# Optimization experiments

Measured on AMD Instinct MI355X. Metric: run time of the kernel, lower is better.

## Reference

```python
import jax, jax.numpy as jnp
import numpy as np

B, L, D = 2, 2048, 2048
H, Hd = 16, 128


def _rotary_cos_sin(max_len, dim, base=10000.0):
    inv_freq = 1.0 / (base ** (np.arange(0, dim, 2, dtype=np.float32) / dim))
    t = np.arange(max_len, dtype=np.float32)
    freqs = np.outer(t, inv_freq)                      # [L, dim/2]
    emb = np.concatenate([freqs, freqs], axis=-1)      # [L, dim]
    cos = np.cos(emb)[None, None]                      # [1,1,L,dim]
    sin = np.sin(emb)[None, None]
    return jnp.asarray(cos), jnp.asarray(sin)


def setup_inputs() -> dict:
    key = jax.random.key(0)
    ks = jax.random.split(key, 5)
    hidden_states = jax.random.normal(ks[0], (B, L, D), dtype=jnp.float32)
    cos, sin = _rotary_cos_sin(L, Hd)
    s = 1.0 / np.sqrt(D)
    wq = jax.random.normal(ks[1], (H * Hd, D), dtype=jnp.float32) * s
    wk = jax.random.normal(ks[2], (H * Hd, D), dtype=jnp.float32) * s
    wv = jax.random.normal(ks[3], (H * Hd, D), dtype=jnp.float32) * s
    wo = jax.random.normal(ks[4], (D, H * Hd), dtype=jnp.float32) * s
    return {"hidden_states": hidden_states, "cos": cos, "sin": sin,
            "wq": wq, "wk": wk, "wv": wv, "wo": wo}


def _rotate_half(x):
    x1, x2 = jnp.split(x, 2, axis=-1)
    return jnp.concatenate([-x2, x1], axis=-1)


def reference(hidden_states, cos, sin, wq, wk, wv, wo):
    b, l, d = hidden_states.shape
    # QKV projections -> [B, H, L, Hd]
    q = (hidden_states @ wq.T).reshape(b, l, H, Hd).transpose(0, 2, 1, 3)
    k = (hidden_states @ wk.T).reshape(b, l, H, Hd).transpose(0, 2, 1, 3)
    v = (hidden_states @ wv.T).reshape(b, l, H, Hd).transpose(0, 2, 1, 3)
    c = cos[:, :, :l, :]
    s = sin[:, :, :l, :]
    q = q * c + _rotate_half(q) * s
    k = k * c + _rotate_half(k) * s
    # SDPA (non-causal, default scale = 1/sqrt(head_dim))
    scale = 1.0 / jnp.sqrt(jnp.asarray(Hd, dtype=q.dtype))
    scores = jnp.einsum('bhqd,bhkd->bhqk', q, k) * scale
    attn = jax.nn.softmax(scores, axis=-1)
    out = jnp.einsum('bhqk,bhkd->bhqd', attn, v)       # [B,H,L,Hd]
    out = out.transpose(0, 2, 1, 3).reshape(b, l, H * Hd)
    return out @ wo.T
```

## Files before the change

kernel.cpp:

```cpp
#include <hip/hip_runtime.h>

constexpr int Bb = 2;
constexpr int Ll = 2048;
constexpr int Dd = 2048;
constexpr int Hh = 16;
constexpr int Hd = 128;
constexpr int M  = Bb * Ll;

typedef __attribute__((ext_vector_type(8)))  short s16x8;
typedef __attribute__((ext_vector_type(4)))  float f32x4;
typedef __attribute__((ext_vector_type(16))) float f32x16;

__device__ __forceinline__ unsigned short f2bf(float f) {
    union { float f; unsigned u; } v; v.f = f;
    unsigned r = v.u + 0x7fffu + ((v.u >> 16) & 1u);
    return (unsigned short)(r >> 16);
}
__device__ __forceinline__ float bf2f(unsigned short b) {
    union { unsigned u; float f; } v; v.u = ((unsigned)b) << 16;
    return v.f;
}
__device__ __forceinline__ float fast_exp2(float x) {
#if __has_builtin(__builtin_amdgcn_exp2f)
    return __builtin_amdgcn_exp2f(x);
#else
    return exp2f(x);
#endif
}

__device__ __forceinline__ void gld16(const void* g, void* l) {
#if __has_builtin(__builtin_amdgcn_global_load_lds)
    __builtin_amdgcn_global_load_lds(
        (const __attribute__((address_space(1))) unsigned int*)g,
        (__attribute__((address_space(3))) unsigned int*)l, 16, 0, 0);
#else
    int lane = threadIdx.x & 63;
    ((int4*)l)[lane] = ((const int4*)g)[0];
#endif
}

__global__ __launch_bounds__(256)
void f2bf_all(const float* __restrict__ x,  const float* __restrict__ wq,
              const float* __restrict__ wk, const float* __restrict__ wv,
              const float* __restrict__ wo,
              unsigned short* __restrict__ Xb,  unsigned short* __restrict__ Wqb,
              unsigned short* __restrict__ Wkb, unsigned short* __restrict__ Wvb,
              unsigned short* __restrict__ Wob)
{
    int bid = blockIdx.x;
    const float* in; unsigned short* out; int off;
    if      (bid <  8192) { in = x;  out = Xb;  off = bid; }
    else if (bid < 12288) { in = wq; out = Wqb; off = bid - 8192; }
    else if (bid < 16384) { in = wk; out = Wkb; off = bid - 12288; }
    else if (bid < 20480) { in = wv; out = Wvb; off = bid - 16384; }
    else                  { in = wo; out = Wob; off = bid - 20480; }
    int i = (off * 256 + threadIdx.x) * 4;
    float4 v = *(const float4*)(in + i);
    ushort4 o;
    o.x = f2bf(v.x); o.y = f2bf(v.y); o.z = f2bf(v.z); o.w = f2bf(v.w);
    *(ushort4*)(out + i) = o;
}

__global__ __launch_bounds__(256, 2)
void mfma_gemm_qkv(const unsigned short* __restrict__ A,
                   const unsigned short* __restrict__ Wall,
                   unsigned short* __restrict__ Oq,
                   unsigned short* __restrict__ Ok,
                   unsigned short* __restrict__ Ov)
{
    constexpr int K  = 2048;
    constexpr int NT = K / 64;
    constexpr int BM = 128, BN = 192;
    constexpr int SLOT_US = (BM + BN) * 64;

    __shared__ unsigned short lds[2 * SLOT_US];

    const int t    = threadIdx.x;
    const int w    = t >> 6, lane = t & 63;
    const int wm   = w >> 1, wn = w & 1;
    const int m0   = blockIdx.y * BM, n0 = blockIdx.x * BN;
    const int r16  = lane & 15, q4 = lane >> 4;
    const int lxor = (r16 & 7) << 4;

    const int srow8 = lane >> 3;
    const int sgcol = (((lane & 7) ^ srow8) << 4);
    const char* Agb = (const char*)A;
    const char* Wgb = (const char*)Wall;

    f32x4 acc[4][6];
#pragma unroll
    for (int i = 0; i < 4; ++i)
#pragma unroll
        for (int j = 0; j < 6; ++j)
            acc[i][j] = (f32x4){0.f, 0.f, 0.f, 0.f};

#define STAGE_ALL(tt, sl) do {                                               \
    _Pragma("unroll") for (int p = 0; p < 4; ++p) {                          \
        int ia_ = w * 4 + p;                                                 \
        gld16(Agb + (size_t)(m0 + ia_ * 8 + srow8) * (K * 2) + (tt) * 128 + sgcol, \
              &lds[(sl) * SLOT_US + ia_ * 512]);                             \
    }                                                                        \
    _Pragma("unroll") for (int p = 0; p < 6; ++p) {                          \
        int ib_ = w * 6 + p;                                                 \
        gld16(Wgb + (size_t)(n0 + ib_ * 8 + srow8) * (K * 2) + (tt) * 128 + sgcol, \
              &lds[(sl) * SLOT_US + BM * 64 + ib_ * 512]);                   \
    }                                                                        \
} while (0)

#define MFMA24() do {                                                        \
    __builtin_amdgcn_s_setprio(1);                                           \
    _Pragma("unroll") for (int mi = 0; mi < 4; ++mi)                         \
    _Pragma("unroll") for (int ni = 0; ni < 6; ++ni)                         \
        acc[mi][ni] = __builtin_amdgcn_mfma_f32_16x16x32_bf16(                \
            a[mi], b[ni], acc[mi][ni], 0, 0, 0);                             \
    __builtin_amdgcn_s_setprio(0);                                           \
} while (0)

    STAGE_ALL(0, 0);
    asm volatile("s_waitcnt vmcnt(0)" ::: "memory");
    __builtin_amdgcn_s_barrier();
    asm volatile("" ::: "memory");

    for (int tt = 0; tt < NT; ++tt) {
        const int slot = tt & 1;
        const char* Ab = (const char*)&lds[slot * SLOT_US];
        const char* Bp = (const char*)&lds[slot * SLOT_US + BM * 64];
        const int c0 = (q4 * 16) ^ lxor;
        const int c1 = (64 + q4 * 16) ^ lxor;

        s16x8 a[4], b[6];

#pragma unroll
        for (int mi = 0; mi < 4; ++mi)
            a[mi] = *(const s16x8*)(Ab + (wm * 64 + mi * 16 + r16) * 128 + c0);
#pragma unroll
        for (int ni = 0; ni < 6; ++ni)
            b[ni] = *(const s16x8*)(Bp + (wn * 96 + ni * 16 + r16) * 128 + c0);
        if (tt + 1 < NT) STAGE_ALL(tt + 1, slot ^ 1);
        MFMA24();

#pragma unroll
        for (int mi = 0; mi < 4; ++mi)
            a[mi] = *(const s16x8*)(Ab + (wm * 64 + mi * 16 + r16) * 128 + c1);
#pragma unroll
        for (int ni = 0; ni < 6; ++ni)
            b[ni] = *(const s16x8*)(Bp + (wn * 96 + ni * 16 + r16) * 128 + c1);
        MFMA24();

        asm volatile("s_waitcnt vmcnt(0)" ::: "memory");
        __builtin_amdgcn_s_barrier();
        asm volatile("" ::: "memory");
    }
#undef STAGE_ALL
#undef MFMA24

#pragma unroll
    for (int ni = 0; ni < 6; ++ni) {
        int nb   = n0 + wn * 96 + ni * 16;
        int nsel = nb >> 11;
        int nr   = nb & 2047;
        int h    = nr >> 7;
        int d    = (nr & 127) + r16;
        if (nsel < 2) {
            unsigned short* O = nsel ? Ok : Oq;
#pragma unroll
            for (int mi = 0; mi < 4; ++mi)
#pragma unroll
                for (int r = 0; r < 4; ++r) {
                    int m = m0 + wm * 64 + mi * 16 + q4 * 4 + r;
                    int b = m >> 11, l = m & 2047;
                    O[(((size_t)b * Hh + h) * Ll + l) * Hd + d] =
                        f2bf(acc[mi][ni][r]);
                }
        } else {
#pragma unroll
            for (int mi = 0; mi < 4; ++mi) {
                int mb = m0 + wm * 64 + mi * 16 + q4 * 4;
                int b = mb >> 11, l = mb & 2047;
                ushort4 pk;
                pk.x = f2bf(acc[mi][ni][0]);
                pk.y = f2bf(acc[mi][ni][1]);
                pk.z = f2bf(acc[mi][ni][2]);
                pk.w = f2bf(acc[mi][ni][3]);
                *(ushort4*)&Ov[(((size_t)b * Hh + h) * Hd + d) * Ll + l] = pk;
            }
        }
    }
}

__global__ __launch_bounds__(512, 2)
void mfma_gemm_out(const unsigned short* __restrict__ A,
                   const unsigned short* __restrict__ W,
                   float* __restrict__ FO)
{
    constexpr int K  = 2048;
    constexpr int NT = K / 64;
    constexpr int SLOT_US = 24576;

    __shared__ unsigned short lds[3 * SLOT_US];

    const int t    = threadIdx.x;
    const int w    = t >> 6, lane = t & 63;
    const int wm   = w >> 1, wn = w & 1;
    const int m0   = blockIdx.y * 256, n0 = blockIdx.x * 128;
    const int r16  = lane & 15, q4 = lane >> 4;
    const int lxor = (r16 & 7) << 4;

    const int srow8 = lane >> 3;
    const int sgcol = (((lane & 7) ^ srow8) << 4);
    const char* Agb = (const char*)A;
    const char* Wgb = (const char*)W;

    f32x4 acc[4][4];
#pragma unroll
    for (int i = 0; i < 4; ++i)
#pragma unroll
        for (int j = 0; j < 4; ++j)
            acc[i][j] = (f32x4){0.f, 0.f, 0.f, 0.f};

    s16x8 af[4], bf[4];

#define STAGE_A(tt, sl, p) do {                                              \
    int ia_ = w * 4 + (p);                                                   \
    gld16(Agb + (size_t)(m0 + ia_ * 8 + srow8) * (K * 2) + (tt) * 128 + sgcol, \
          &lds[(sl) * SLOT_US + ia_ * 512]); } while (0)
#define STAGE_B(tt, sl, p) do {                                              \
    int ib_ = w * 2 + (p);                                                   \
    gld16(Wgb + (size_t)(n0 + ib_ * 8 + srow8) * (K * 2) + (tt) * 128 + sgcol, \
          &lds[(sl) * SLOT_US + 16384 + ib_ * 512]); } while (0)

#define LOAD_FRAGS(sl, ksub) do {                                            \
    const char* Ab_ = (const char*)&lds[(sl) * SLOT_US];                     \
    const char* Bb_ = (const char*)&lds[(sl) * SLOT_US + 16384];             \
    int cc_ = ((ksub) * 64 + q4 * 16) ^ lxor;                                \
    _Pragma("unroll") for (int mi = 0; mi < 4; ++mi)                         \
        af[mi] = *(const s16x8*)(Ab_ + (wm * 64 + mi * 16 + r16) * 128 + cc_); \
    _Pragma("unroll") for (int ni = 0; ni < 4; ++ni)                         \
        bf[ni] = *(const s16x8*)(Bb_ + (wn * 64 + ni * 16 + r16) * 128 + cc_); \
} while (0)

#define DO_MFMA() do {                                                       \
    __builtin_amdgcn_s_setprio(1);                                           \
    _Pragma("unroll") for (int mi = 0; mi < 4; ++mi)                         \
    _Pragma("unroll") for (int ni = 0; ni < 4; ++ni)                         \
        acc[mi][ni] = __builtin_amdgcn_mfma_f32_16x16x32_bf16(                \
            af[mi], bf[ni], acc[mi][ni], 0, 0, 0);                           \
    __builtin_amdgcn_s_setprio(0);                                           \
} while (0)

    STAGE_A(0, 0, 0); STAGE_A(0, 0, 1); STAGE_B(0, 0, 0);
    STAGE_A(0, 0, 2); STAGE_A(0, 0, 3); STAGE_B(0, 0, 1);
    STAGE_A(1, 1, 0); STAGE_A(1, 1, 1); STAGE_B(1, 1, 0);
    STAGE_A(1, 1, 2); STAGE_A(1, 1, 3); STAGE_B(1, 1, 1);
    asm volatile("s_waitcnt vmcnt(6)" ::: "memory");
    __builtin_amdgcn_s_barrier();
    asm volatile("" ::: "memory");

    int slot = 0;
    for (int tt = 0; tt < NT; ++tt) {
        int snx = slot + 2; if (snx >= 3) snx -= 3;
        const bool pf = (tt + 2 < NT);

        LOAD_FRAGS(slot, 0);
        if (pf) { STAGE_A(tt + 2, snx, 0); STAGE_A(tt + 2, snx, 1); STAGE_B(tt + 2, snx, 0); }
        asm volatile("" ::: "memory");
        __builtin_amdgcn_s_barrier();
        asm volatile("s_waitcnt lgkmcnt(0)" ::: "memory");
        DO_MFMA();
        asm volatile("" ::: "memory");
        __builtin_amdgcn_s_barrier();
        asm volatile("" ::: "memory");

        LOAD_FRAGS(slot, 1);
        if (pf) { STAGE_A(tt + 2, snx, 2); STAGE_A(tt + 2, snx, 3); STAGE_B(tt + 2, snx, 1); }
        asm volatile("" ::: "memory");
        __builtin_amdgcn_s_barrier();
        asm volatile("s_waitcnt lgkmcnt(0)" ::: "memory");
        DO_MFMA();
        if (pf)               asm volatile("s_waitcnt vmcnt(6)" ::: "memory");
        else if (tt + 1 < NT) asm volatile("s_waitcnt vmcnt(0)" ::: "memory");
        asm volatile("" ::: "memory");
        __builtin_amdgcn_s_barrier();
        asm volatile("" ::: "memory");

        slot = (slot == 2) ? 0 : slot + 1;
    }
#undef STAGE_A
#undef STAGE_B
#undef LOAD_FRAGS
#undef DO_MFMA

#pragma unroll
    for (int mi = 0; mi < 4; ++mi)
#pragma unroll
        for (int ni = 0; ni < 4; ++ni) {
            int n = n0 + wn * 64 + ni * 16 + r16;
#pragma unroll
            for (int r = 0; r < 4; ++r) {
                int m = m0 + wm * 64 + mi * 16 + q4 * 4 + r;
                FO[(size_t)m * Dd + n] = acc[mi][ni][r];
            }
        }
}

__global__ __launch_bounds__(256)
void rope_bf16(unsigned short* __restrict__ q, unsigned short* __restrict__ k,
               const float* __restrict__ cosb, const float* __restrict__ sinb)
{
    const float QS = 0.1275175f;
    const int t = threadIdx.x;
    int rblk = blockIdx.x;
    unsigned short* base;
    float sc;
    if (rblk < 4096) { base = q; sc = QS; }
    else             { base = k; sc = 1.0f; rblk -= 4096; }

    const int row = rblk * 16 + (t >> 4);
    const int l   = row & (Ll - 1);
    const int d0  = (t & 15) * 8;
    unsigned short* xr = base + (size_t)row * Hd;

    s16x8 v0 = *(const s16x8*)(xr + d0);
    s16x8 vp = *(const s16x8*)(xr + (d0 ^ 64));
    const float* cp = cosb + (size_t)l * Hd + d0;
    const float* sp = sinb + (size_t)l * Hd + d0;
    float4 c0 = *(const float4*)cp,       c1 = *(const float4*)(cp + 4);
    float4 sa = *(const float4*)sp,       sb = *(const float4*)(sp + 4);
    const float cc[8] = {c0.x, c0.y, c0.z, c0.w, c1.x, c1.y, c1.z, c1.w};
    const float ss[8] = {sa.x, sa.y, sa.z, sa.w, sb.x, sb.y, sb.z, sb.w};
    const float sgn = (d0 < 64) ? -1.f : 1.f;

    s16x8 o;
#pragma unroll
    for (int j = 0; j < 8; ++j) {
        float a = bf2f((unsigned short)v0[j]);
        float p = bf2f((unsigned short)vp[j]);
        float res = fmaf(a, cc[j], sgn * p * ss[j]) * sc;
        o[j] = (short)f2bf(res);
    }
    asm volatile("" ::: "memory");
    *(s16x8*)(xr + d0) = o;
}

__global__ __launch_bounds__(256)
void flash_attn(const unsigned short* __restrict__ q,
                const unsigned short* __restrict__ k,
                const unsigned short* __restrict__ vT,
                unsigned short* __restrict__ ctx)
{
    __shared__ unsigned short Ks[2][64 * 128];
    __shared__ unsigned short Vs[2][128 * 64];
    __shared__ unsigned short Ps[4][32 * 64];

    const int t = threadIdx.x;
    const int w = t >> 6, lane = t & 63;
    const int n32 = lane & 31, half = lane >> 5;
    const int bh = blockIdx.x >> 4;
    const int l0 = (blockIdx.x & 15) * 128;

    const unsigned short* qb = q  + ((size_t)bh * Ll + l0 + w * 32) * Hd;
    const unsigned short* kb = k  + (size_t)bh * Ll * Hd;
    const unsigned short* vb = vT + (size_t)bh * Hd * Ll;

    const int k_r = lane >> 4, k_u = lane & 15;
    const int v_r = lane >> 3, v_u = lane & 7;

#define STAGE(J0, bsel) do {                                                  \
    _Pragma("unroll") for (int p = 0; p < 4; ++p) {                           \
        int j_ = w * 4 + p;                                                   \
        int row_ = j_ * 4 + k_r;                                              \
        gld16(kb + (size_t)((J0) + row_) * Hd + ((k_u ^ (row_ & 7)) * 8),     \
              &Ks[bsel][j_ * 512]);                                           \
    }                                                                         \
    _Pragma("unroll") for (int p = 0; p < 4; ++p) {                           \
        int j_ = w * 4 + p;                                                   \
        int row_ = j_ * 8 + v_r;                                              \
        gld16(vb + (size_t)row_ * Ll + (J0) + ((v_u ^ (row_ & 7)) * 8),       \
              &Vs[bsel][j_ * 512]);                                           \
    }                                                                         \
} while (0)

    s16x8 qf[8];
#pragma unroll
    for (int ks = 0; ks < 8; ++ks)
        qf[ks] = *(const s16x8*)(qb + (size_t)n32 * Hd + ks * 16 + half * 8);

    f32x16 o[4];
    float lacc[16];
#pragma unroll
    for (int nt = 0; nt < 4; ++nt)
#pragma unroll
        for (int r = 0; r < 16; ++r) o[nt][r] = 0.f;
#pragma unroll
    for (int r = 0; r < 16; ++r) lacc[r] = 0.f;

    unsigned short* Pw = Ps[w];
    const int psw = (n32 & 7) << 3;

    STAGE(0, 0);
    __syncthreads();

    int buf = 0;
    for (int j0 = 0; j0 < Ll; j0 += 64) {
        if (j0 + 64 < Ll) STAGE(j0 + 64, buf ^ 1);

        f32x16 s0, s1;
#pragma unroll
        for (int r = 0; r < 16; ++r) { s0[r] = 0.f; s1[r] = 0.f; }
        __builtin_amdgcn_s_setprio(1);
#pragma unroll
        for (int ks = 0; ks < 8; ++ks) {
            int kc = (ks * 16 + half * 8) ^ psw;
            s16x8 b0 = *(const s16x8*)&Ks[buf][n32 * 128 + kc];
            s16x8 b1 = *(const s16x8*)&Ks[buf][(32 + n32) * 128 + kc];
            s0 = __builtin_amdgcn_mfma_f32_32x32x16_bf16(qf[ks], b0, s0, 0, 0, 0);
            s1 = __builtin_amdgcn_mfma_f32_32x32x16_bf16(qf[ks], b1, s1, 0, 0, 0);
        }
        __builtin_amdgcn_s_setprio(0);

#pragma unroll
        for (int r = 0; r < 16; ++r) {
            int mrow = (r & 3) + 8 * (r >> 2) + 4 * half;
            int sw = (mrow & 7) << 3;
            float p0 = fast_exp2(s0[r]);
            float p1 = fast_exp2(s1[r]);
            lacc[r] += p0 + p1;
            union { float f; unsigned u; } u0, u1;
            u0.f = p0; u1.f = p1;
            Pw[mrow * 64 + (n32 ^ sw)]        = (unsigned short)((u0.u + 0x8000u) >> 16);
            Pw[mrow * 64 + ((32 + n32) ^ sw)] = (unsigned short)((u1.u + 0x8000u) >> 16);
        }

        __builtin_amdgcn_s_setprio(1);
#pragma unroll
        for (int kst = 0; kst < 4; ++kst) {
            int cc = (kst * 16 + half * 8) ^ psw;
            s16x8 pf2 = *(const s16x8*)&Pw[n32 * 64 + cc];
#pragma unroll
            for (int nt = 0; nt < 4; ++nt) {
                s16x8 vf = *(const s16x8*)&Vs[buf][(nt * 32 + n32) * 64 + cc];
                o[nt] = __builtin_amdgcn_mfma_f32_32x32x16_bf16(pf2, vf, o[nt], 0, 0, 0);
            }
        }
        __builtin_amdgcn_s_setprio(0);

        __syncthreads();
        buf ^= 1;
    }
#undef STAGE

    float linv[16];
#pragma unroll
    for (int r = 0; r < 16; ++r) {
        float s = lacc[r];
        s += __shfl_xor(s, 1, 64);
        s += __shfl_xor(s, 2, 64);
        s += __shfl_xor(s, 4, 64);
        s += __shfl_xor(s, 8, 64);
        s += __shfl_xor(s, 16, 64);
        linv[r] = 1.0f / s;
    }

    const int b = bh >> 4, h = bh & 15;
#pragma unroll
    for (int nt = 0; nt < 4; ++nt)
#pragma unroll
        for (int r = 0; r < 16; ++r) {
            int mrow = (r & 3) + 8 * (r >> 2) + 4 * half;
            int lq = l0 + w * 32 + mrow;
            ctx[((size_t)(b * Ll + lq)) * Dd + h * Hd + nt * 32 + n32] =
                f2bf(o[nt][r] * linv[r]);
        }
}

extern "C" void kernel_launch(void* const* d_in, const int* in_sizes, int n_in,
                              void* d_out, int out_size, void* d_ws, size_t ws_size,
                              hipStream_t stream)
{
    const float* hs   = (const float*)d_in[0];
    const float* cosb = (const float*)d_in[1];
    const float* sinb = (const float*)d_in[2];
    const float* wq   = (const float*)d_in[3];
    const float* wk   = (const float*)d_in[4];
    const float* wv   = (const float*)d_in[5];
    const float* wo   = (const float*)d_in[6];
    float* out = (float*)d_out;

    char* ws = (char*)d_ws;
    unsigned short* Xb  = (unsigned short*)(ws);
    unsigned short* Wqb = (unsigned short*)(ws + (16ull << 20));
    unsigned short* Wkb = (unsigned short*)(ws + (24ull << 20));
    unsigned short* Wvb = (unsigned short*)(ws + (32ull << 20));
    unsigned short* Wob = (unsigned short*)(ws + (40ull << 20));
    unsigned short* qb  = (unsigned short*)(ws + (48ull << 20));
    unsigned short* kb  = (unsigned short*)(ws + (64ull << 20));
    unsigned short* vTb = (unsigned short*)(ws + (80ull << 20));
    unsigned short* ctx = Xb;

    f2bf_all<<<dim3(24576), dim3(256), 0, stream>>>(
        hs, wq, wk, wv, wo, Xb, Wqb, Wkb, Wvb, Wob);

    mfma_gemm_qkv<<<dim3(6144 / 192, M / 128), dim3(256), 0, stream>>>(
        Xb, Wqb, qb, kb, vTb);

    rope_bf16<<<dim3(2 * (Bb * Hh * Ll) / 16), dim3(256), 0, stream>>>(
        qb, kb, cosb, sinb);

    flash_attn<<<dim3(Bb * Hh * (Ll / 128)), dim3(256), 0, stream>>>(qb, kb, vTb, ctx);

    mfma_gemm_out<<<dim3(Dd / 128, M / 256), dim3(512), 0, stream>>>(
        ctx, Wob, out);
}
```

Measured before the change: 386.2 us.

## Load QKV GEMM A fragments directly from global into registers, drop A LDS staging

The QKV projection GEMM no longer stages the activation tile through LDS. Each wave now loads its A fragments straight from global memory into double-buffered registers one tile ahead, and only the weight tile goes through LDS. This shrinks LDS per block and raises the launch-bounds occupancy hint from 2 to 3 blocks, and the barrier wait now only covers the B-tile loads (vmcnt(8)). The trade-off is higher register pressure from the two sets of 8 A fragments, and global loads that are less coalesced, with each lane reading 16-byte pieces spread across rows.

```diff
diff --git a/kernel.cpp b/kernel.cpp
--- a/kernel.cpp
+++ b/kernel.cpp
@@ -61,7 +61,7 @@
     *(ushort4*)(out + i) = o;
 }
 
-__global__ __launch_bounds__(256, 2)
+__global__ __launch_bounds__(256, 3)
 void mfma_gemm_qkv(const unsigned short* __restrict__ A,
                    const unsigned short* __restrict__ Wall,
                    unsigned short* __restrict__ Oq,
@@ -71,7 +71,7 @@
     constexpr int K  = 2048;
     constexpr int NT = K / 64;
     constexpr int BM = 128, BN = 192;
-    constexpr int SLOT_US = (BM + BN) * 64;
+    constexpr int SLOT_US = BN * 64;
 
     __shared__ unsigned short lds[2 * SLOT_US];
 
@@ -87,6 +87,9 @@
     const char* Agb = (const char*)A;
     const char* Wgb = (const char*)Wall;
 
+    const int c0 = (q4 * 16) ^ lxor;
+    const int c1 = (64 + q4 * 16) ^ lxor;
+
     f32x4 acc[4][6];
 #pragma unroll
     for (int i = 0; i < 4; ++i)
@@ -94,65 +97,70 @@
         for (int j = 0; j < 6; ++j)
             acc[i][j] = (f32x4){0.f, 0.f, 0.f, 0.f};
 
-#define STAGE_ALL(tt, sl) do {                                               \
-    _Pragma("unroll") for (int p = 0; p < 4; ++p) {                          \
-        int ia_ = w * 4 + p;                                                 \
-        gld16(Agb + (size_t)(m0 + ia_ * 8 + srow8) * (K * 2) + (tt) * 128 + sgcol, \
-              &lds[(sl) * SLOT_US + ia_ * 512]);                             \
-    }                                                                        \
+#define STAGE_B(tt, sl) do {                                                 \
     _Pragma("unroll") for (int p = 0; p < 6; ++p) {                          \
         int ib_ = w * 6 + p;                                                 \
         gld16(Wgb + (size_t)(n0 + ib_ * 8 + srow8) * (K * 2) + (tt) * 128 + sgcol, \
-              &lds[(sl) * SLOT_US + BM * 64 + ib_ * 512]);                   \
+              &lds[(sl) * SLOT_US + ib_ * 512]);                             \
+    } } while (0)
+
+#define AFRAG_LOAD(dst, tt) do {                                             \
+    _Pragma("unroll") for (int mi = 0; mi < 4; ++mi) {                       \
+        const char* ap_ = Agb + (size_t)(m0 + wm * 64 + mi * 16 + r16) * (K * 2) \
+                          + (tt) * 128 + q4 * 16;                            \
+        dst[mi]     = *(const s16x8*)(ap_);                                  \
+        dst[4 + mi] = *(const s16x8*)(ap_ + 64);                             \
+    } } while (0)
+
+#define TILE(tt, aC, aN) do {                                                \
+    const int sl_ = (tt) & 1;                                                \
+    if ((tt) + 1 < NT) {                                                     \
+        STAGE_B((tt) + 1, sl_ ^ 1);                                          \
+        asm volatile("" ::: "memory");       \
+        AFRAG_LOAD(aN, (tt) + 1);                                            \
+        asm volatile("" ::: "memory");                                       \
     }                                                                        \
-} while (0)
-
-#define MFMA24() do {                                                        \
+    const char* Bp_ = (const char*)&lds[sl_ * SLOT_US];                      \
+    s16x8 bf_[6];                                                            \
+    _Pragma("unroll") for (int ni = 0; ni < 6; ++ni)                         \
+        bf_[ni] = *(const s16x8*)(Bp_ + (wn * 96 + ni * 16 + r16) * 128 + c0); \
     __builtin_amdgcn_s_setprio(1);                                           \
     _Pragma("unroll") for (int mi = 0; mi < 4; ++mi)                         \
     _Pragma("unroll") for (int ni = 0; ni < 6; ++ni)                         \
         acc[mi][ni] = __builtin_amdgcn_mfma_f32_16x16x32_bf16(                \
-            a[mi], b[ni], acc[mi][ni], 0, 0, 0);                             \
+            aC[mi], bf_[ni], acc[mi][ni], 0, 0, 0);                          \
     __builtin_amdgcn_s_setprio(0);                                           \
+    _Pragma("unroll") for (int ni = 0; ni < 6; ++ni)                         \
+        bf_[ni] = *(const s16x8*)(Bp_ + (wn * 96 + ni * 16 + r16) * 128 + c1); \
+    __builtin_amdgcn_s_setprio(1);                                           \
+    _Pragma("unroll") for (int mi = 0; mi < 4; ++mi)                         \
+    _Pragma("unroll") for (int ni = 0; ni < 6; ++ni)                         \
+        acc[mi][ni] = __builtin_amdgcn_mfma_f32_16x16x32_bf16(                \
+            aC[4 + mi], bf_[ni], acc[mi][ni], 0, 0, 0);                      \
+    __builtin_amdgcn_s_setprio(0);                                           \
+    if ((tt) + 1 < NT) {                                                     \
+        asm volatile("s_waitcnt vmcnt(8)" ::: "memory");   \
+        __builtin_amdgcn_s_barrier();                                        \
+        asm volatile("" ::: "memory");                                       \
+    }                                                                        \
 } while (0)
 
-    STAGE_ALL(0, 0);
+    s16x8 aA[8], aB[8];
+
+    STAGE_B(0, 0);
+    AFRAG_LOAD(aA, 0);
     asm volatile("s_waitcnt vmcnt(0)" ::: "memory");
     __builtin_amdgcn_s_barrier();
     asm volatile("" ::: "memory");
 
-    for (int tt = 0; tt < NT; ++tt) {
-        const int slot = tt & 1;
-        const char* Ab = (const char*)&lds[slot * SLOT_US];
-        const char* Bp = (const char*)&lds[slot * SLOT_US + BM * 64];
-        const int c0 = (q4 * 16) ^ lxor;
-        const int c1 = (64 + q4 * 16) ^ lxor;
-
-        s16x8 a[4], b[6];
-
-#pragma unroll
-        for (int mi = 0; mi < 4; ++mi)
-            a[mi] = *(const s16x8*)(Ab + (wm * 64 + mi * 16 + r16) * 128 + c0);
-#pragma unroll
-        for (int ni = 0; ni < 6; ++ni)
-            b[ni] = *(const s16x8*)(Bp + (wn * 96 + ni * 16 + r16) * 128 + c0);
-        if (tt + 1 < NT) STAGE_ALL(tt + 1, slot ^ 1);
-        MFMA24();
-
-#pragma unroll
-        for (int mi = 0; mi < 4; ++mi)
-            a[mi] = *(const s16x8*)(Ab + (wm * 64 + mi * 16 + r16) * 128 + c1);
-#pragma unroll
-        for (int ni = 0; ni < 6; ++ni)
-            b[ni] = *(const s16x8*)(Bp + (wn * 96 + ni * 16 + r16) * 128 + c1);
-        MFMA24();
-
-        asm volatile("s_waitcnt vmcnt(0)" ::: "memory");
-        __builtin_amdgcn_s_barrier();
-        asm volatile("" ::: "memory");
+#pragma unroll 1
+    for (int it = 0; it < NT; it += 2) {
+        TILE(it,     aA, aB);
+        TILE(it + 1, aB, aA);
     }
-#undef STAGE_ALL
-#undef MFMA24
+#undef STAGE_B
+#undef AFRAG_LOAD
+#undef TILE
 
 #pragma unroll
     for (int ni = 0; ni < 6; ++ni) {
```

Measured after the change: 959.6 us. 148% more time.

## Process two query tiles per wave in flash attention to reuse K/V

Applied to the files above, without the earlier changes.

Each wave now handles 64 query rows (two 32-row tiles) instead of 32, so every block covers 256 queries and the grid halves. Each K and V fragment read from LDS feeds twice as many MFMAs, and K/V global traffic per query is halved. In exchange register pressure roughly doubles (launch bounds set to 1 block per SM), the P scratch buffer grows, and only 256 blocks are launched, which may underfill the GPU's compute units.

```diff
diff --git a/kernel.cpp b/kernel.cpp
--- a/kernel.cpp
+++ b/kernel.cpp
@@ -342,7 +342,7 @@
     *(s16x8*)(xr + d0) = o;
 }
 
-__global__ __launch_bounds__(256)
+__global__ __launch_bounds__(256, 1)
 void flash_attn(const unsigned short* __restrict__ q,
                 const unsigned short* __restrict__ k,
                 const unsigned short* __restrict__ vT,
@@ -350,15 +350,15 @@
 {
     __shared__ unsigned short Ks[2][64 * 128];
     __shared__ unsigned short Vs[2][128 * 64];
-    __shared__ unsigned short Ps[4][32 * 64];
+    __shared__ unsigned short Ps[8][32 * 64];
 
     const int t = threadIdx.x;
     const int w = t >> 6, lane = t & 63;
     const int n32 = lane & 31, half = lane >> 5;
-    const int bh = blockIdx.x >> 4;
-    const int l0 = (blockIdx.x & 15) * 128;
-
-    const unsigned short* qb = q  + ((size_t)bh * Ll + l0 + w * 32) * Hd;
+    const int bh = blockIdx.x >> 3;
+    const int l0 = (blockIdx.x & 7) * 256;
+
+    const unsigned short* qb = q  + ((size_t)bh * Ll + l0) * Hd;
     const unsigned short* kb = k  + (size_t)bh * Ll * Hd;
     const unsigned short* vb = vT + (size_t)bh * Hd * Ll;
 
@@ -380,21 +380,24 @@
     }                                                                         \
 } while (0)
 
-    s16x8 qf[8];
-#pragma unroll
-    for (int ks = 0; ks < 8; ++ks)
-        qf[ks] = *(const s16x8*)(qb + (size_t)n32 * Hd + ks * 16 + half * 8);
-
-    f32x16 o[4];
-    float lacc[16];
+    s16x8 qf0[8], qf1[8];
+#pragma unroll
+    for (int ks = 0; ks < 8; ++ks) {
+        qf0[ks] = *(const s16x8*)(qb + (size_t)((w * 2 + 0) * 32 + n32) * Hd + ks * 16 + half * 8);
+        qf1[ks] = *(const s16x8*)(qb + (size_t)((w * 2 + 1) * 32 + n32) * Hd + ks * 16 + half * 8);
+    }
+
+    f32x16 o0[4], o1[4];
+    float la0[16], la1[16];
 #pragma unroll
     for (int nt = 0; nt < 4; ++nt)
 #pragma unroll
-        for (int r = 0; r < 16; ++r) o[nt][r] = 0.f;
-#pragma unroll
-    for (int r = 0; r < 16; ++r) lacc[r] = 0.f;
-
-    unsigned short* Pw = Ps[w];
+        for (int r = 0; r < 16; ++r) { o0[nt][r] = 0.f; o1[nt][r] = 0.f; }
+#pragma unroll
+    for (int r = 0; r < 16; ++r) { la0[r] = 0.f; la1[r] = 0.f; }
+
+    unsigned short* Pw0 = Ps[w * 2 + 0];
+    unsigned short* Pw1 = Ps[w * 2 + 1];
     const int psw = (n32 & 7) << 3;
 
     STAGE(0, 0);
@@ -404,17 +407,19 @@
     for (int j0 = 0; j0 < Ll; j0 += 64) {
         if (j0 + 64 < Ll) STAGE(j0 + 64, buf ^ 1);
 
-        f32x16 s0, s1;
-#pragma unroll
-        for (int r = 0; r < 16; ++r) { s0[r] = 0.f; s1[r] = 0.f; }
+        f32x16 s00, s01, s10, s11;
+#pragma unroll
+        for (int r = 0; r < 16; ++r) { s00[r] = 0.f; s01[r] = 0.f; s10[r] = 0.f; s11[r] = 0.f; }
         __builtin_amdgcn_s_setprio(1);
 #pragma unroll
         for (int ks = 0; ks < 8; ++ks) {
             int kc = (ks * 16 + half * 8) ^ psw;
             s16x8 b0 = *(const s16x8*)&Ks[buf][n32 * 128 + kc];
             s16x8 b1 = *(const s16x8*)&Ks[buf][(32 + n32) * 128 + kc];
-            s0 = __builtin_amdgcn_mfma_f32_32x32x16_bf16(qf[ks], b0, s0, 0, 0, 0);
-            s1 = __builtin_amdgcn_mfma_f32_32x32x16_bf16(qf[ks], b1, s1, 0, 0, 0);
+            s00 = __builtin_amdgcn_mfma_f32_32x32x16_bf16(qf0[ks], b0, s00, 0, 0, 0);
+            s01 = __builtin_amdgcn_mfma_f32_32x32x16_bf16(qf0[ks], b1, s01, 0, 0, 0);
+            s10 = __builtin_amdgcn_mfma_f32_32x32x16_bf16(qf1[ks], b0, s10, 0, 0, 0);
+            s11 = __builtin_amdgcn_mfma_f32_32x32x16_bf16(qf1[ks], b1, s11, 0, 0, 0);
         }
         __builtin_amdgcn_s_setprio(0);
 
@@ -422,24 +427,31 @@
         for (int r = 0; r < 16; ++r) {
             int mrow = (r & 3) + 8 * (r >> 2) + 4 * half;
             int sw = (mrow & 7) << 3;
-            float p0 = fast_exp2(s0[r]);
-            float p1 = fast_exp2(s1[r]);
-            lacc[r] += p0 + p1;
-            union { float f; unsigned u; } u0, u1;
-            u0.f = p0; u1.f = p1;
-            Pw[mrow * 64 + (n32 ^ sw)]        = (unsigned short)((u0.u + 0x8000u) >> 16);
-            Pw[mrow * 64 + ((32 + n32) ^ sw)] = (unsigned short)((u1.u + 0x8000u) >> 16);
+            float p00 = fast_exp2(s00[r]);
+            float p01 = fast_exp2(s01[r]);
+            float p10 = fast_exp2(s10[r]);
+            float p11 = fast_exp2(s11[r]);
+            la0[r] += p00 + p01;
+            la1[r] += p10 + p11;
+            union { float f; unsigned u; } u0, u1, u2, u3;
+            u0.f = p00; u1.f = p01; u2.f = p10; u3.f = p11;
+            Pw0[mrow * 64 + (n32 ^ sw)]        = (unsigned short)((u0.u + 0x8000u) >> 16);
+            Pw0[mrow * 64 + ((32 + n32) ^ sw)] = (unsigned short)((u1.u + 0x8000u) >> 16);
+            Pw1[mrow * 64 + (n32 ^ sw)]        = (unsigned short)((u2.u + 0x8000u) >> 16);
+            Pw1[mrow * 64 + ((32 + n32) ^ sw)] = (unsigned short)((u3.u + 0x8000u) >> 16);
         }
 
         __builtin_amdgcn_s_setprio(1);
 #pragma unroll
         for (int kst = 0; kst < 4; ++kst) {
             int cc = (kst * 16 + half * 8) ^ psw;
-            s16x8 pf2 = *(const s16x8*)&Pw[n32 * 64 + cc];
+            s16x8 pa = *(const s16x8*)&Pw0[n32 * 64 + cc];
+            s16x8 pb = *(const s16x8*)&Pw1[n32 * 64 + cc];
 #pragma unroll
             for (int nt = 0; nt < 4; ++nt) {
                 s16x8 vf = *(const s16x8*)&Vs[buf][(nt * 32 + n32) * 64 + cc];
-                o[nt] = __builtin_amdgcn_mfma_f32_32x32x16_bf16(pf2, vf, o[nt], 0, 0, 0);
+                o0[nt] = __builtin_amdgcn_mfma_f32_32x32x16_bf16(pa, vf, o0[nt], 0, 0, 0);
+                o1[nt] = __builtin_amdgcn_mfma_f32_32x32x16_bf16(pb, vf, o1[nt], 0, 0, 0);
             }
         }
         __builtin_amdgcn_s_setprio(0);
@@ -449,16 +461,23 @@
     }
 #undef STAGE
 
-    float linv[16];
+    float li0[16], li1[16];
 #pragma unroll
     for (int r = 0; r < 16; ++r) {
-        float s = lacc[r];
+        float s = la0[r];
         s += __shfl_xor(s, 1, 64);
         s += __shfl_xor(s, 2, 64);
         s += __shfl_xor(s, 4, 64);
         s += __shfl_xor(s, 8, 64);
         s += __shfl_xor(s, 16, 64);
-        linv[r] = 1.0f / s;
+        li0[r] = 1.0f / s;
+        float z = la1[r];
+        z += __shfl_xor(z, 1, 64);
+        z += __shfl_xor(z, 2, 64);
+        z += __shfl_xor(z, 4, 64);
+        z += __shfl_xor(z, 8, 64);
+        z += __shfl_xor(z, 16, 64);
+        li1[r] = 1.0f / z;
     }
 
     const int b = bh >> 4, h = bh & 15;
@@ -467,9 +486,12 @@
 #pragma unroll
         for (int r = 0; r < 16; ++r) {
             int mrow = (r & 3) + 8 * (r >> 2) + 4 * half;
-            int lq = l0 + w * 32 + mrow;
-            ctx[((size_t)(b * Ll + lq)) * Dd + h * Hd + nt * 32 + n32] =
-                f2bf(o[nt][r] * linv[r]);
+            int lq0 = l0 + (w * 2 + 0) * 32 + mrow;
+            int lq1 = l0 + (w * 2 + 1) * 32 + mrow;
+            ctx[((size_t)(b * Ll + lq0)) * Dd + h * Hd + nt * 32 + n32] =
+                f2bf(o0[nt][r] * li0[r]);
+            ctx[((size_t)(b * Ll + lq1)) * Dd + h * Hd + nt * 32 + n32] =
+                f2bf(o1[nt][r] * li1[r]);
         }
 }
 
@@ -506,7 +528,7 @@
     rope_bf16<<<dim3(2 * (Bb * Hh * Ll) / 16), dim3(256), 0, stream>>>(
         qb, kb, cosb, sinb);
 
-    flash_attn<<<dim3(Bb * Hh * (Ll / 128)), dim3(256), 0, stream>>>(qb, kb, vTb, ctx);
+    flash_attn<<<dim3(Bb * Hh * (Ll / 256)), dim3(256), 0, stream>>>(qb, kb, vTb, ctx);
 
     mfma_gemm_out<<<dim3(Dd / 128, M / 256), dim3(512), 0, stream>>>(
         ctx, Wob, out);
```

Result: slower. 408.7 us (+5.8%).

## Shrink output GEMM tile to 128x128 with double-buffered LDS pipeline

Applied to the files above, without the earlier changes.

Changes the output projection GEMM from 256x128 tiles with 512 threads and a triple-buffered, two-barrier-per-half-step pipeline to 128x128 tiles with 256 threads and a simple double-buffered loop with one barrier per K step. This doubles the grid size (512 blocks) to improve CU occupancy and cuts synchronisation overhead. In exchange, prefetch depth drops to one stage with a full vmcnt(0) wait each iteration, and the smaller tile gives less data reuse per block.

```diff
diff --git a/kernel.cpp b/kernel.cpp
--- a/kernel.cpp
+++ b/kernel.cpp
@@ -188,21 +188,22 @@
     }
 }
 
-__global__ __launch_bounds__(512, 2)
+__global__ __launch_bounds__(256, 2)
 void mfma_gemm_out(const unsigned short* __restrict__ A,
                    const unsigned short* __restrict__ W,
                    float* __restrict__ FO)
 {
     constexpr int K  = 2048;
     constexpr int NT = K / 64;
-    constexpr int SLOT_US = 24576;
-
-    __shared__ unsigned short lds[3 * SLOT_US];
+    constexpr int BM = 128, BN = 128;
+    constexpr int SLOT_US = (BM + BN) * 64;
+
+    __shared__ unsigned short lds[2 * SLOT_US];
 
     const int t    = threadIdx.x;
     const int w    = t >> 6, lane = t & 63;
     const int wm   = w >> 1, wn = w & 1;
-    const int m0   = blockIdx.y * 256, n0 = blockIdx.x * 128;
+    const int m0   = blockIdx.y * BM, n0 = blockIdx.x * BN;
     const int r16  = lane & 15, q4 = lane >> 4;
     const int lxor = (r16 & 7) << 4;
 
@@ -218,77 +219,65 @@
         for (int j = 0; j < 4; ++j)
             acc[i][j] = (f32x4){0.f, 0.f, 0.f, 0.f};
 
-    s16x8 af[4], bf[4];
-
-#define STAGE_A(tt, sl, p) do {                                              \
-    int ia_ = w * 4 + (p);                                                   \
-    gld16(Agb + (size_t)(m0 + ia_ * 8 + srow8) * (K * 2) + (tt) * 128 + sgcol, \
-          &lds[(sl) * SLOT_US + ia_ * 512]); } while (0)
-#define STAGE_B(tt, sl, p) do {                                              \
-    int ib_ = w * 2 + (p);                                                   \
-    gld16(Wgb + (size_t)(n0 + ib_ * 8 + srow8) * (K * 2) + (tt) * 128 + sgcol, \
-          &lds[(sl) * SLOT_US + 16384 + ib_ * 512]); } while (0)
-
-#define LOAD_FRAGS(sl, ksub) do {                                            \
-    const char* Ab_ = (const char*)&lds[(sl) * SLOT_US];                     \
-    const char* Bb_ = (const char*)&lds[(sl) * SLOT_US + 16384];             \
-    int cc_ = ((ksub) * 64 + q4 * 16) ^ lxor;                                \
-    _Pragma("unroll") for (int mi = 0; mi < 4; ++mi)                         \
-        af[mi] = *(const s16x8*)(Ab_ + (wm * 64 + mi * 16 + r16) * 128 + cc_); \
-    _Pragma("unroll") for (int ni = 0; ni < 4; ++ni)                         \
-        bf[ni] = *(const s16x8*)(Bb_ + (wn * 64 + ni * 16 + r16) * 128 + cc_); \
+#define STAGE_ALL(tt, sl) do {                                               \
+    _Pragma("unroll") for (int p = 0; p < 4; ++p) {                          \
+        int ia_ = w * 4 + p;                                                 \
+        gld16(Agb + (size_t)(m0 + ia_ * 8 + srow8) * (K * 2) + (tt) * 128 + sgcol, \
+              &lds[(sl) * SLOT_US + ia_ * 512]);                             \
+    }                                                                        \
+    _Pragma("unroll") for (int p = 0; p < 4; ++p) {                          \
+        int ib_ = w * 4 + p;                                                 \
+        gld16(Wgb + (size_t)(n0 + ib_ * 8 + srow8) * (K * 2) + (tt) * 128 + sgcol, \
+              &lds[(sl) * SLOT_US + BM * 64 + ib_ * 512]);                   \
+    }                                                                        \
 } while (0)
 
-#define DO_MFMA() do {                                                       \
+#define MFMA16() do {                                                        \
     __builtin_amdgcn_s_setprio(1);                                           \
     _Pragma("unroll") for (int mi = 0; mi < 4; ++mi)                         \
     _Pragma("unroll") for (int ni = 0; ni < 4; ++ni)                         \
         acc[mi][ni] = __builtin_amdgcn_mfma_f32_16x16x32_bf16(                \
-            af[mi], bf[ni], acc[mi][ni], 0, 0, 0);                           \
+            a[mi], b[ni], acc[mi][ni], 0, 0, 0);                             \
     __builtin_amdgcn_s_setprio(0);                                           \
 } while (0)
 
-    STAGE_A(0, 0, 0); STAGE_A(0, 0, 1); STAGE_B(0, 0, 0);
-    STAGE_A(0, 0, 2); STAGE_A(0, 0, 3); STAGE_B(0, 0, 1);
-    STAGE_A(1, 1, 0); STAGE_A(1, 1, 1); STAGE_B(1, 1, 0);
-    STAGE_A(1, 1, 2); STAGE_A(1, 1, 3); STAGE_B(1, 1, 1);
-    asm volatile("s_waitcnt vmcnt(6)" ::: "memory");
+    STAGE_ALL(0, 0);
+    asm volatile("s_waitcnt vmcnt(0)" ::: "memory");
     __builtin_amdgcn_s_barrier();
     asm volatile("" ::: "memory");
 
-    int slot = 0;
     for (int tt = 0; tt < NT; ++tt) {
-        int snx = slot + 2; if (snx >= 3) snx -= 3;
-        const bool pf = (tt + 2 < NT);
-
-        LOAD_FRAGS(slot, 0);
-        if (pf) { STAGE_A(tt + 2, snx, 0); STAGE_A(tt + 2, snx, 1); STAGE_B(tt + 2, snx, 0); }
-        asm volatile("" ::: "memory");
-        __builtin_amdgcn_s_barrier();
-        asm volatile("s_waitcnt lgkmcnt(0)" ::: "memory");
-        DO_MFMA();
-        asm volatile("" ::: "memory");
+        const int slot = tt & 1;
+        const char* Ab = (const char*)&lds[slot * SLOT_US];
+        const char* Bp = (const char*)&lds[slot * SLOT_US + BM * 64];
+        const int c0 = (q4 * 16) ^ lxor;
+        const int c1 = (64 + q4 * 16) ^ lxor;
+
+        s16x8 a[4], b[4];
+
+#pragma unroll
+        for (int mi = 0; mi < 4; ++mi)
+            a[mi] = *(const s16x8*)(Ab + (wm * 64 + mi * 16 + r16) * 128 + c0);
+#pragma unroll
+        for (int ni = 0; ni < 4; ++ni)
+            b[ni] = *(const s16x8*)(Bp + (wn * 64 + ni * 16 + r16) * 128 + c0);
+        if (tt + 1 < NT) STAGE_ALL(tt + 1, slot ^ 1);
+        MFMA16();
+
+#pragma unroll
+        for (int mi = 0; mi < 4; ++mi)
+            a[mi] = *(const s16x8*)(Ab + (wm * 64 + mi * 16 + r16) * 128 + c1);
+#pragma unroll
+        for (int ni = 0; ni < 4; ++ni)
+            b[ni] = *(const s16x8*)(Bp + (wn * 64 + ni * 16 + r16) * 128 + c1);
+        MFMA16();
+
+        asm volatile("s_waitcnt vmcnt(0)" ::: "memory");
         __builtin_amdgcn_s_barrier();
         asm volatile("" ::: "memory");
-
-        LOAD_FRAGS(slot, 1);
-        if (pf) { STAGE_A(tt + 2, snx, 2); STAGE_A(tt + 2, snx, 3); STAGE_B(tt + 2, snx, 1); }
-        asm volatile("" ::: "memory");
-        __builtin_amdgcn_s_barrier();
-        asm volatile("s_waitcnt lgkmcnt(0)" ::: "memory");
-        DO_MFMA();
-        if (pf)               asm volatile("s_waitcnt vmcnt(6)" ::: "memory");
-        else if (tt + 1 < NT) asm volatile("s_waitcnt vmcnt(0)" ::: "memory");
-        asm volatile("" ::: "memory");
-        __builtin_amdgcn_s_barrier();
-        asm volatile("" ::: "memory");
-
-        slot = (slot == 2) ? 0 : slot + 1;
     }
-#undef STAGE_A
-#undef STAGE_B
-#undef LOAD_FRAGS
-#undef DO_MFMA
+#undef STAGE_ALL
+#undef MFMA16
 
 #pragma unroll
     for (int mi = 0; mi < 4; ++mi)
@@ -508,6 +497,6 @@
 
     flash_attn<<<dim3(Bb * Hh * (Ll / 128)), dim3(256), 0, stream>>>(qb, kb, vTb, ctx);
 
-    mfma_gemm_out<<<dim3(Dd / 128, M / 256), dim3(512), 0, stream>>>(
+    mfma_gemm_out<<<dim3(Dd / 128, M / 128), dim3(256), 0, stream>>>(
         ctx, Wob, out);
 }
```

Result: no change. 379.6 us (-1.7%).
